# Optimization experiments

Hardware: AMD Instinct MI355X
Metric: run time of the kernel (lower is better)

The kernel has to match this reference:

```python
import jax, jax.numpy as jnp
import numpy as np

HIDDEN = 64
HALF = 32
VOCAB = 64
B, L = 256, 2048


def _l2norm(x):
    # matches torch F.normalize(dim=-1, eps=1e-12)
    return x / jnp.maximum(jnp.linalg.norm(x, axis=-1, keepdims=True), 1e-12)


def setup_inputs() -> dict:
    key = jax.random.key(0)
    ks = jax.random.split(key, 16)
    s = 0.02
    return {
        "seq": jax.random.randint(ks[0], (B, L), 0, VOCAB),
        "embed": jax.random.normal(ks[1], (VOCAB, HIDDEN), jnp.float32) * s,
        "W1": jax.random.normal(ks[2], (2 * HIDDEN, HIDDEN), jnp.float32) * s,
        "b1": jnp.zeros((2 * HIDDEN,), jnp.float32),
        "W2": jax.random.normal(ks[3], (HIDDEN, 2 * HIDDEN), jnp.float32) * s,
        "b2": jnp.zeros((HIDDEN,), jnp.float32),
        "ln_g": jnp.ones((HIDDEN,), jnp.float32),
        "ln_b": jnp.zeros((HIDDEN,), jnp.float32),
        "Ws": jax.random.normal(ks[4], (HALF, HIDDEN), jnp.float32) * s,
        "bs": jnp.zeros((HALF,), jnp.float32),
        "We": jax.random.normal(ks[5], (HALF, HIDDEN), jnp.float32) * s,
        "be": jnp.zeros((HALF,), jnp.float32),
        "Wrp": jax.random.normal(ks[6], (HIDDEN, 2 * HALF), jnp.float32) * s,
        "brp": jnp.zeros((HIDDEN,), jnp.float32),
        "Wo": jax.random.normal(ks[7], (VOCAB, HIDDEN), jnp.float32) * s,
        "bo": jnp.zeros((VOCAB,), jnp.float32),
    }


def reference(seq, embed, W1, b1, W2, b2, ln_g, ln_b, Ws, bs, We, be, Wrp, brp, Wo, bo):
    # Encoder: embed -> LayerNorm(h + FF(h))
    h0 = embed[seq]                                     # [B,L,H]
    ff = jnp.maximum(h0 @ W1.T + b1, 0.0) @ W2.T + b2
    x = h0 + ff
    mu = x.mean(-1, keepdims=True)
    var = x.var(-1, keepdims=True)
    h = (x - mu) / jnp.sqrt(var + 1e-5) * ln_g + ln_b   # [B,L,H]

    Bn, Ln, _ = h.shape
    half = Ws.shape[0]
    hs_all = h @ Ws.T + bs                              # [B,L,half]
    he_all = h @ We.T + be

    # sequential delta-rule memory writes over t = 0 .. L-2
    hs_seq = jnp.swapaxes(hs_all[:, :-1], 0, 1)         # [L-1,B,half]
    he_seq = jnp.swapaxes(he_all[:, :-1], 0, 1)
    scales = (jnp.arange(1, Ln) / Ln).astype(h.dtype)   # (t+1)/L
    M0 = jnp.zeros((Bn, half, half), h.dtype)

    def step(carry, inp):
        M_s, M_e = carry
        hs, he, sc = inp
        ks_ = _l2norm(hs)
        ke_ = _l2norm(he)
        vps = jnp.einsum('bij,bj->bi', M_s, ks_)
        vpe = jnp.einsum('bij,bj->bi', M_e, ke_)
        M_s = M_s + (hs - vps)[:, :, None] * ks_[:, None, :]
        M_e = M_e + sc * (he - vpe)[:, :, None] * ke_[:, None, :]
        return (M_s, M_e), None

    (M_s, M_e), _ = jax.lax.scan(step, (M0, M0), (hs_seq, he_seq, scales))

    # read with last-position query
    qs = _l2norm(hs_all[:, -1])
    qe = _l2norm(he_all[:, -1])
    rs = jnp.einsum('bij,bj->bi', M_s, qs)
    re = jnp.einsum('bij,bj->bi', M_e, qe)
    r = jnp.concatenate([rs, re], axis=-1)              # [B, 2*half]
    return (r @ Wrp.T + brp) @ Wo.T + bo                # [B, vocab]
```

## Files before the change

### kernel.cpp

```cpp
#include <hip/hip_runtime.h>

#define HIDDEN 64
#define HALFD  32
#define VOCAB  64
#define BATCH  256
#define SEQLEN 2048

#define RLF(v, sl) __int_as_float(__builtin_amdgcn_readlane(__float_as_int(v), (sl)))
#define RLI(v, sl) __builtin_amdgcn_readlane((v), (sl))
#define GIX(j,m) (((j)==0?0:(j)==1?7:(j)==2?13:(j)==3?18:(j)==4?22:(j)==5?25:27) + (m) - (j) - 1)
#define OM(m) (((m)*((m)+1))>>1)

__global__ __launch_bounds__(64) void vocab_kernel(
    const float* __restrict__ embed, const float* __restrict__ W1, const float* __restrict__ b1,
    const float* __restrict__ W2, const float* __restrict__ b2,
    const float* __restrict__ ln_g, const float* __restrict__ ln_b,
    const float* __restrict__ Ws, const float* __restrict__ bs,
    const float* __restrict__ We, const float* __restrict__ be,
    float* __restrict__ ws)
{
    const int v = blockIdx.x;
    const int tid = threadIdx.x;

    __shared__ float e_s[64];
    __shared__ float a1_s[128];
    __shared__ float h_s[64];

    e_s[tid] = embed[v * 64 + tid];
    __syncthreads();

    float acc0 = b1[tid], acc1 = b1[tid + 64];
    #pragma unroll 8
    for (int m = 0; m < 64; ++m) {
        float ev = e_s[m];
        acc0 = fmaf(ev, W1[tid * 64 + m], acc0);
        acc1 = fmaf(ev, W1[(tid + 64) * 64 + m], acc1);
    }
    a1_s[tid]      = fmaxf(acc0, 0.0f);
    a1_s[tid + 64] = fmaxf(acc1, 0.0f);
    __syncthreads();

    float ff = b2[tid];
    #pragma unroll 8
    for (int m = 0; m < 128; ++m) ff = fmaf(a1_s[m], W2[tid * 128 + m], ff);
    float x = e_s[tid] + ff;

    float s = x, s2 = x * x;
    #pragma unroll
    for (int off = 32; off >= 1; off >>= 1) {
        s  += __shfl_xor(s,  off, 64);
        s2 += __shfl_xor(s2, off, 64);
    }
    float mu  = s * (1.0f / 64.0f);
    float var = s2 * (1.0f / 64.0f) - mu * mu;
    float hval = (x - mu) * rsqrtf(var + 1e-5f) * ln_g[tid] + ln_b[tid];
    h_s[tid] = hval;
    __syncthreads();

    const int j = tid & 31;
    const bool is_s = tid < 32;
    const float* W = is_s ? Ws : We;
    float acc = is_s ? bs[j] : be[j];
    #pragma unroll 8
    for (int m = 0; m < 64; ++m) acc = fmaf(h_s[m], W[j * 64 + m], acc);

    float n2 = acc * acc;
    #pragma unroll
    for (int off = 16; off >= 1; off >>= 1) n2 += __shfl_xor(n2, off, 64);
    float norm = sqrtf(n2);
    float kn = acc / fmaxf(norm, 1e-12f);

    const int base = v * 32 + j;
    if (is_s) { ws[base]        = kn; ws[4096 + base] = acc; }
    else      { ws[2048 + base] = kn; ws[6144 + base] = acc; }
}

__global__ __launch_bounds__(256) void gram_kernel(float* __restrict__ ws)
{
    const int w = blockIdx.x;
    const int tid = threadIdx.x;
    __shared__ float k_s[2048];
    const float* kb = ws + w * 2048;
    for (int i = tid; i < 2048; i += 256) k_s[i] = kb[i];
    __syncthreads();
    const int a  = tid >> 2;
    const int b0 = (tid & 3) << 4;
    float* Gw = ws + 8192 + w * 4096 + a * 64;
    for (int bb = 0; bb < 16; ++bb) {
        const int bcol = b0 + bb;
        float acc = 0.f;
        #pragma unroll
        for (int m = 0; m < 32; ++m) acc = fmaf(k_s[a * 32 + m], k_s[bcol * 32 + m], acc);
        Gw[bcol] = acc;
    }
}

static __device__ __forceinline__ void build_wpack(
    const int* tj, float fb, float invL, bool is_e, bool is_last, float* Wp,
    const float* __restrict__ Gg)
{
    float f[8];
    #pragma unroll
    for (int j = 0; j < 8; ++j) f[j] = is_e ? (fb + (float)j * invL) : 1.0f;
    if (is_last) f[7] = 0.0f;

    float g[28];
    #pragma unroll
    for (int j = 0; j < 7; ++j)
        #pragma unroll
        for (int m = j + 1; m < 8; ++m) g[GIX(j, m)] = Gg[tj[j] * 64 + tj[m]];

    #pragma unroll
    for (int m = 0; m < 8; ++m) {
        float col[8];
        col[m] = f[m];
        #pragma unroll
        for (int j = 6; j >= 0; --j) {
            if (j < m) {
                float acc = 0.0f;
                #pragma unroll
                for (int p = 1; p < 8; ++p)
                    if (p > j && p <= m) acc = fmaf(g[GIX(j, p)], col[p], acc);
                col[j] = -f[j] * acc;
            }
        }
        #pragma unroll
        for (int j = 0; j < 8; ++j)
            if (j <= m) Wp[OM(m) + j] = col[j];
    }
}

struct Chunk {
    int   tokv;
    int   tk[8];
    float grow[8];
    float W[36];
};

__global__ __launch_bounds__(128) void scan_kernel(
    const int* __restrict__ seq, const float* __restrict__ ws,
    const float* __restrict__ Wrp, const float* __restrict__ brp,
    const float* __restrict__ Wo, const float* __restrict__ bo,
    float* __restrict__ out)
{
    const int b    = blockIdx.x;
    const int tid  = threadIdx.x;
    const int w    = tid >> 6;
    const int lane = tid & 63;
    const int l7   = lane & 7;
    const bool is_e = (w == 1);

    __shared__ __align__(16) float4 Wt4[9][2][256];
    __shared__ __align__(16) int    toklds[SEQLEN];
    __shared__ float wacc_s[2][64];
    __shared__ float r_s[64];
    __shared__ float t1_s[64];

    const float* Gg = ws + 8192 + w * 4096;
    const int*   sq = seq + b * SEQLEN;

    {
        const int4* sq4 = (const int4*)sq;
        int4* tl = (int4*)toklds;
        #pragma unroll
        for (int i = 0; i < 4; ++i) tl[tid + i * 128] = sq4[tid + i * 128];
    }
    __syncthreads();

    {
        const float invL = 1.0f / (float)SEQLEN;
        #pragma unroll
        for (int qq = 0; qq < 4; ++qq) {
            const int c = lane + (qq << 6);
            int tj[8];
            #pragma unroll
            for (int j = 0; j < 8; ++j) tj[j] = toklds[c * 8 + j];
            float Wp[36];
            build_wpack(tj, (float)(8 * c + 1) * invL, invL, is_e, c == 255, Wp, Gg);
            #pragma unroll
            for (int i = 0; i < 9; ++i)
                Wt4[i][w][c] = make_float4(Wp[4*i], Wp[4*i+1], Wp[4*i+2], Wp[4*i+3]);
        }
    }
    __syncthreads();

    Chunk A, B;
    float u, waccv = 0.0f;

    A.tokv = sq[2040 + l7];
    #pragma unroll
    for (int j = 0; j < 8; ++j) A.tk[j] = RLI(A.tokv, j);
    #pragma unroll
    for (int j = 0; j < 8; ++j) A.grow[j] = Gg[A.tk[j] * 64 + lane];
    #pragma unroll
    for (int i = 0; i < 9; ++i) {
        float4 v = Wt4[i][w][255];
        A.W[4*i] = v.x; A.W[4*i+1] = v.y; A.W[4*i+2] = v.z; A.W[4*i+3] = v.w;
    }
    B.tokv = sq[2032 + l7];
    u = Gg[A.tk[7] * 64 + lane];
    float braw = __shfl(u, A.tokv, 64);

    auto body = [&](Chunk& cur, Chunk& nxt, int c) {
        float t0 = RLF(braw, 0), t1 = RLF(braw, 1), t2 = RLF(braw, 2), t3 = RLF(braw, 3);
        float t4 = RLF(braw, 4), t5 = RLF(braw, 5), t6 = RLF(braw, 6), t7 = RLF(braw, 7);

        const int cm1 = (c > 0) ? c - 1 : 0;
        const int cm2 = (c > 1) ? c - 2 : 0;
        #pragma unroll
        for (int j = 0; j < 8; ++j) nxt.tk[j] = RLI(nxt.tokv, j);
        #pragma unroll
        for (int j = 0; j < 8; ++j) nxt.grow[j] = Gg[nxt.tk[j] * 64 + lane];
        #pragma unroll
        for (int i = 0; i < 9; ++i) {
            float4 v = Wt4[i][w][cm1];
            nxt.W[4*i] = v.x; nxt.W[4*i+1] = v.y; nxt.W[4*i+2] = v.z; nxt.W[4*i+3] = v.w;
        }
        int tokv2 = sq[cm2 * 8 + l7];

        const float* W = cur.W;
        float s7 = W[35] * t7;
        float s6 = fmaf(W[27], t6, W[34] * t7);
        float s5 = fmaf(W[20], t5, W[26] * t6) + W[33] * t7;
        float s4 = fmaf(W[14], t4, W[19] * t5) + fmaf(W[25], t6, W[32] * t7);
        float s3 = fmaf(W[9],  t3, W[13] * t4) + fmaf(W[18], t5, fmaf(W[24], t6, W[31] * t7));
        float s2 = fmaf(W[5],  t2, W[8]  * t3) + fmaf(W[12], t4, W[17] * t5) + fmaf(W[23], t6, W[30] * t7);
        float s1 = fmaf(W[2],  t1, W[4]  * t2) + fmaf(W[7],  t3, W[11] * t4) + fmaf(W[16], t5, fmaf(W[22], t6, W[29] * t7));
        float s0 = fmaf(W[0],  t0, W[1]  * t1) + fmaf(W[3],  t2, W[6]  * t3) + fmaf(W[10], t4, W[15] * t5) + fmaf(W[21], t6, W[28] * t7);

        float dA = fmaf(cur.grow[0], s0, fmaf(cur.grow[1], s1, fmaf(cur.grow[2], s2, cur.grow[3] * s3)));
        float dB = fmaf(cur.grow[4], s4, fmaf(cur.grow[5], s5, fmaf(cur.grow[6], s6, cur.grow[7] * s7)));
        u -= (dA + dB);

        braw = __shfl(u, nxt.tokv, 64);

        waccv += (lane == cur.tk[0]) ? s0 : 0.0f;
        waccv += (lane == cur.tk[1]) ? s1 : 0.0f;
        waccv += (lane == cur.tk[2]) ? s2 : 0.0f;
        waccv += (lane == cur.tk[3]) ? s3 : 0.0f;
        waccv += (lane == cur.tk[4]) ? s4 : 0.0f;
        waccv += (lane == cur.tk[5]) ? s5 : 0.0f;
        waccv += (lane == cur.tk[6]) ? s6 : 0.0f;
        waccv += (lane == cur.tk[7]) ? s7 : 0.0f;

        cur.tokv = tokv2;
    };

    for (int c = 255; c >= 1; c -= 2) {
        body(A, B, c);
        body(B, A, c - 1);
    }

    wacc_s[w][lane] = waccv;
    __syncthreads();

    if (tid < 64) {
        const int w2  = tid >> 5;
        const int rho = tid & 31;
        const float* vv = ws + 4096 + w2 * 2048;
        const float* wa = &wacc_s[w2][0];
        float acc = 0.0f;
        #pragma unroll 8
        for (int tok = 0; tok < 64; ++tok) acc = fmaf(wa[tok], vv[tok * 32 + rho], acc);
        r_s[tid] = acc;
    }
    __syncthreads();

    if (tid < 64) {
        float acc = brp[tid];
        #pragma unroll 8
        for (int m = 0; m < 64; ++m) acc = fmaf(Wrp[tid * 64 + m], r_s[m], acc);
        t1_s[tid] = acc;
    }
    __syncthreads();
    if (tid < 64) {
        float acc = bo[tid];
        #pragma unroll 8
        for (int m = 0; m < 64; ++m) acc = fmaf(Wo[tid * 64 + m], t1_s[m], acc);
        out[b * 64 + tid] = acc;
    }
}

extern "C" void kernel_launch(void* const* d_in, const int* in_sizes, int n_in,
                              void* d_out, int out_size, void* d_ws, size_t ws_size,
                              hipStream_t stream)
{
    const int*   seq   = (const int*)  d_in[0];
    const float* embed = (const float*)d_in[1];
    const float* W1    = (const float*)d_in[2];
    const float* b1    = (const float*)d_in[3];
    const float* W2    = (const float*)d_in[4];
    const float* b2    = (const float*)d_in[5];
    const float* ln_g  = (const float*)d_in[6];
    const float* ln_b  = (const float*)d_in[7];
    const float* Ws    = (const float*)d_in[8];
    const float* bs    = (const float*)d_in[9];
    const float* We    = (const float*)d_in[10];
    const float* be    = (const float*)d_in[11];
    const float* Wrp   = (const float*)d_in[12];
    const float* brp   = (const float*)d_in[13];
    const float* Wo    = (const float*)d_in[14];
    const float* bo    = (const float*)d_in[15];
    float* ws  = (float*)d_ws;
    float* out = (float*)d_out;

    hipLaunchKernelGGL(vocab_kernel, dim3(VOCAB), dim3(64), 0, stream,
                       embed, W1, b1, W2, b2, ln_g, ln_b, Ws, bs, We, be, ws);
    hipLaunchKernelGGL(gram_kernel, dim3(2), dim3(256), 0, stream, ws);
    hipLaunchKernelGGL(scan_kernel, dim3(BATCH), dim3(128), 0, stream,
                       seq, ws, Wrp, brp, Wo, bo, out);
}
```

Measured before the change: 200.6 us.

## Restructure chunked scan recurrence with lookahead correction and lane-parallel triangular solve

The scan loop now spreads the 8x8 triangular chunk solve across lanes: each lane holds one row of the solve matrix, stored in LDS in an XOR-swizzled layout, and the results are broadcast with readlane. The next chunk's input is gathered one step early and then corrected with the previous chunk's outputs, which takes the shuffle off the serial dependency chain. The gram kernel is split over more blocks with padded shared memory, and the small matvec loops use multiple accumulators to increase ILP. In exchange the loop does extra shuffles per step and the floating-point summation order changes.

New measurement: 190.6 us. -5.0%, faster.

```diff
diff --git a/kernel.cpp b/kernel.cpp
--- a/kernel.cpp
+++ b/kernel.cpp
@@ -29,21 +29,32 @@
     e_s[tid] = embed[v * 64 + tid];
     __syncthreads();
 
-    float acc0 = b1[tid], acc1 = b1[tid + 64];
-    #pragma unroll 8
-    for (int m = 0; m < 64; ++m) {
-        float ev = e_s[m];
-        acc0 = fmaf(ev, W1[tid * 64 + m], acc0);
-        acc1 = fmaf(ev, W1[(tid + 64) * 64 + m], acc1);
-    }
-    a1_s[tid]      = fmaxf(acc0, 0.0f);
-    a1_s[tid + 64] = fmaxf(acc1, 0.0f);
-    __syncthreads();
-
-    float ff = b2[tid];
-    #pragma unroll 8
-    for (int m = 0; m < 128; ++m) ff = fmaf(a1_s[m], W2[tid * 128 + m], ff);
-    float x = e_s[tid] + ff;
+    float p0 = b1[tid], p1 = 0.f, p2 = 0.f, p3 = 0.f;
+    float q0 = b1[tid + 64], q1 = 0.f, q2 = 0.f, q3 = 0.f;
+    #pragma unroll
+    for (int m = 0; m < 64; m += 4) {
+        p0 = fmaf(e_s[m],   W1[tid * 64 + m],     p0);
+        p1 = fmaf(e_s[m+1], W1[tid * 64 + m + 1], p1);
+        p2 = fmaf(e_s[m+2], W1[tid * 64 + m + 2], p2);
+        p3 = fmaf(e_s[m+3], W1[tid * 64 + m + 3], p3);
+        q0 = fmaf(e_s[m],   W1[(tid + 64) * 64 + m],     q0);
+        q1 = fmaf(e_s[m+1], W1[(tid + 64) * 64 + m + 1], q1);
+        q2 = fmaf(e_s[m+2], W1[(tid + 64) * 64 + m + 2], q2);
+        q3 = fmaf(e_s[m+3], W1[(tid + 64) * 64 + m + 3], q3);
+    }
+    a1_s[tid]      = fmaxf((p0 + p1) + (p2 + p3), 0.0f);
+    a1_s[tid + 64] = fmaxf((q0 + q1) + (q2 + q3), 0.0f);
+    __syncthreads();
+
+    float f0 = b2[tid], f1 = 0.f, f2 = 0.f, f3 = 0.f;
+    #pragma unroll
+    for (int m = 0; m < 128; m += 4) {
+        f0 = fmaf(a1_s[m],   W2[tid * 128 + m],     f0);
+        f1 = fmaf(a1_s[m+1], W2[tid * 128 + m + 1], f1);
+        f2 = fmaf(a1_s[m+2], W2[tid * 128 + m + 2], f2);
+        f3 = fmaf(a1_s[m+3], W2[tid * 128 + m + 3], f3);
+    }
+    float x = e_s[tid] + ((f0 + f1) + (f2 + f3));
 
     float s = x, s2 = x * x;
     #pragma unroll
@@ -60,9 +71,16 @@
     const int j = tid & 31;
     const bool is_s = tid < 32;
     const float* W = is_s ? Ws : We;
-    float acc = is_s ? bs[j] : be[j];
-    #pragma unroll 8
-    for (int m = 0; m < 64; ++m) acc = fmaf(h_s[m], W[j * 64 + m], acc);
+    float c0 = is_s ? bs[j] : be[j];
+    float c1 = 0.f, c2 = 0.f, c3 = 0.f;
+    #pragma unroll
+    for (int m = 0; m < 64; m += 4) {
+        c0 = fmaf(h_s[m],   W[j * 64 + m],     c0);
+        c1 = fmaf(h_s[m+1], W[j * 64 + m + 1], c1);
+        c2 = fmaf(h_s[m+2], W[j * 64 + m + 2], c2);
+        c3 = fmaf(h_s[m+3], W[j * 64 + m + 3], c3);
+    }
+    float acc = (c0 + c1) + (c2 + c3);
 
     float n2 = acc * acc;
     #pragma unroll
@@ -77,21 +95,26 @@
 
 __global__ __launch_bounds__(256) void gram_kernel(float* __restrict__ ws)
 {
-    const int w = blockIdx.x;
+    const int w   = blockIdx.x & 1;
+    const int seg = blockIdx.x >> 1;
     const int tid = threadIdx.x;
-    __shared__ float k_s[2048];
+    __shared__ float k_s[64][33];
     const float* kb = ws + w * 2048;
-    for (int i = tid; i < 2048; i += 256) k_s[i] = kb[i];
-    __syncthreads();
-    const int a  = tid >> 2;
-    const int b0 = (tid & 3) << 4;
+    for (int i = tid; i < 2048; i += 256) k_s[i >> 5][i & 31] = kb[i];
+    __syncthreads();
+    const int a  = seg * 16 + (tid >> 4);
+    const int b0 = (tid & 15) << 2;
     float* Gw = ws + 8192 + w * 4096 + a * 64;
-    for (int bb = 0; bb < 16; ++bb) {
+    #pragma unroll
+    for (int bb = 0; bb < 4; ++bb) {
         const int bcol = b0 + bb;
-        float acc = 0.f;
-        #pragma unroll
-        for (int m = 0; m < 32; ++m) acc = fmaf(k_s[a * 32 + m], k_s[bcol * 32 + m], acc);
-        Gw[bcol] = acc;
+        float acc0 = 0.f, acc1 = 0.f;
+        #pragma unroll
+        for (int m = 0; m < 32; m += 2) {
+            acc0 = fmaf(k_s[a][m],     k_s[bcol][m],     acc0);
+            acc1 = fmaf(k_s[a][m + 1], k_s[bcol][m + 1], acc1);
+        }
+        Gw[bcol] = acc0 + acc1;
     }
 }
 
@@ -134,7 +157,9 @@
     int   tokv;
     int   tk[8];
     float grow[8];
-    float W[36];
+    float R[8];
+    float braw;
+    float bp[8];
 };
 
 __global__ __launch_bounds__(128) void scan_kernel(
@@ -150,8 +175,8 @@
     const int l7   = lane & 7;
     const bool is_e = (w == 1);
 
-    __shared__ __align__(16) float4 Wt4[9][2][256];
-    __shared__ __align__(16) int    toklds[SEQLEN];
+    __shared__ __align__(16) float Wlds[2][256][8][8];
+    __shared__ __align__(16) int   toklds[SEQLEN];
     __shared__ float wacc_s[2][64];
     __shared__ float r_s[64];
     __shared__ float t1_s[64];
@@ -177,73 +202,100 @@
             for (int j = 0; j < 8; ++j) tj[j] = toklds[c * 8 + j];
             float Wp[36];
             build_wpack(tj, (float)(8 * c + 1) * invL, invL, is_e, c == 255, Wp, Gg);
+            const int cx = c & 7;
             #pragma unroll
-            for (int i = 0; i < 9; ++i)
-                Wt4[i][w][c] = make_float4(Wp[4*i], Wp[4*i+1], Wp[4*i+2], Wp[4*i+3]);
+            for (int i = 0; i < 8; ++i) {
+                float r[8];
+                #pragma unroll
+                for (int m = 0; m < 8; ++m) r[m] = (m >= i) ? Wp[OM(m) + i] : 0.0f;
+                float4* dst = (float4*)&Wlds[w][c][i ^ cx][0];
+                dst[0] = make_float4(r[0], r[1], r[2], r[3]);
+                dst[1] = make_float4(r[4], r[5], r[6], r[7]);
+            }
         }
     }
     __syncthreads();
 
     Chunk A, B;
-    float u, waccv = 0.0f;
+    float u, wacc0 = 0.0f, wacc1 = 0.0f;
+    float sp0, sp1, sp2, sp3, sp4, sp5, sp6, sp7;
 
     A.tokv = sq[2040 + l7];
+    B.tokv = sq[2032 + l7];
+    int tv2 = sq[2024 + l7];
     #pragma unroll
     for (int j = 0; j < 8; ++j) A.tk[j] = RLI(A.tokv, j);
     #pragma unroll
     for (int j = 0; j < 8; ++j) A.grow[j] = Gg[A.tk[j] * 64 + lane];
-    #pragma unroll
-    for (int i = 0; i < 9; ++i) {
-        float4 v = Wt4[i][w][255];
-        A.W[4*i] = v.x; A.W[4*i+1] = v.y; A.W[4*i+2] = v.z; A.W[4*i+3] = v.w;
-    }
-    B.tokv = sq[2032 + l7];
+    {
+        const float4* rp = (const float4*)&Wlds[w][255][l7 ^ 7][0];
+        float4 lo = rp[0], hi = rp[1];
+        A.R[0] = lo.x; A.R[1] = lo.y; A.R[2] = lo.z; A.R[3] = lo.w;
+        A.R[4] = hi.x; A.R[5] = hi.y; A.R[6] = hi.z; A.R[7] = hi.w;
+    }
     u = Gg[A.tk[7] * 64 + lane];
-    float braw = __shfl(u, A.tokv, 64);
+    A.braw = __shfl(u, A.tokv, 64);
+    B.braw = __shfl(u, B.tokv, 64);
+    #pragma unroll
+    for (int j = 0; j < 8; ++j) {
+        A.bp[j] = 0.0f;
+        B.bp[j] = __shfl(A.grow[j], B.tokv, 64);
+    }
+    sp0 = sp1 = sp2 = sp3 = sp4 = sp5 = sp6 = sp7 = 0.0f;
 
     auto body = [&](Chunk& cur, Chunk& nxt, int c) {
-        float t0 = RLF(braw, 0), t1 = RLF(braw, 1), t2 = RLF(braw, 2), t3 = RLF(braw, 3);
-        float t4 = RLF(braw, 4), t5 = RLF(braw, 5), t6 = RLF(braw, 6), t7 = RLF(braw, 7);
-
         const int cm1 = (c > 0) ? c - 1 : 0;
-        const int cm2 = (c > 1) ? c - 2 : 0;
+        const int cm3 = (c > 2) ? c - 3 : 0;
+
+        float c01 = fmaf(cur.bp[1], sp1, cur.bp[0] * sp0);
+        float c23 = fmaf(cur.bp[3], sp3, cur.bp[2] * sp2);
+        float c45 = fmaf(cur.bp[5], sp5, cur.bp[4] * sp4);
+        float c67 = fmaf(cur.bp[7], sp7, cur.bp[6] * sp6);
+        float tl = cur.braw - ((c01 + c23) + (c45 + c67));
+        float t0 = RLF(tl, 0), t1 = RLF(tl, 1), t2 = RLF(tl, 2), t3 = RLF(tl, 3);
+        float t4 = RLF(tl, 4), t5 = RLF(tl, 5), t6 = RLF(tl, 6), t7 = RLF(tl, 7);
+
         #pragma unroll
         for (int j = 0; j < 8; ++j) nxt.tk[j] = RLI(nxt.tokv, j);
         #pragma unroll
         for (int j = 0; j < 8; ++j) nxt.grow[j] = Gg[nxt.tk[j] * 64 + lane];
-        #pragma unroll
-        for (int i = 0; i < 9; ++i) {
-            float4 v = Wt4[i][w][cm1];
-            nxt.W[4*i] = v.x; nxt.W[4*i+1] = v.y; nxt.W[4*i+2] = v.z; nxt.W[4*i+3] = v.w;
+        {
+            const float4* rp = (const float4*)&Wlds[w][cm1][l7 ^ (cm1 & 7)][0];
+            float4 lo = rp[0], hi = rp[1];
+            nxt.R[0] = lo.x; nxt.R[1] = lo.y; nxt.R[2] = lo.z; nxt.R[3] = lo.w;
+            nxt.R[4] = hi.x; nxt.R[5] = hi.y; nxt.R[6] = hi.z; nxt.R[7] = hi.w;
         }
-        int tokv2 = sq[cm2 * 8 + l7];
-
-        const float* W = cur.W;
-        float s7 = W[35] * t7;
-        float s6 = fmaf(W[27], t6, W[34] * t7);
-        float s5 = fmaf(W[20], t5, W[26] * t6) + W[33] * t7;
-        float s4 = fmaf(W[14], t4, W[19] * t5) + fmaf(W[25], t6, W[32] * t7);
-        float s3 = fmaf(W[9],  t3, W[13] * t4) + fmaf(W[18], t5, fmaf(W[24], t6, W[31] * t7));
-        float s2 = fmaf(W[5],  t2, W[8]  * t3) + fmaf(W[12], t4, W[17] * t5) + fmaf(W[23], t6, W[30] * t7);
-        float s1 = fmaf(W[2],  t1, W[4]  * t2) + fmaf(W[7],  t3, W[11] * t4) + fmaf(W[16], t5, fmaf(W[22], t6, W[29] * t7));
-        float s0 = fmaf(W[0],  t0, W[1]  * t1) + fmaf(W[3],  t2, W[6]  * t3) + fmaf(W[10], t4, W[15] * t5) + fmaf(W[21], t6, W[28] * t7);
+        int tv3 = sq[cm3 * 8 + l7];
+
+        const float* R = cur.R;
+        float a0 = fmaf(R[1], t1, R[0] * t0);
+        float a1 = fmaf(R[3], t3, R[2] * t2);
+        float a2 = fmaf(R[5], t5, R[4] * t4);
+        float a3 = fmaf(R[7], t7, R[6] * t6);
+        float sd = (a0 + a1) + (a2 + a3);
+        float s0 = RLF(sd, 0), s1 = RLF(sd, 1), s2 = RLF(sd, 2), s3 = RLF(sd, 3);
+        float s4 = RLF(sd, 4), s5 = RLF(sd, 5), s6 = RLF(sd, 6), s7 = RLF(sd, 7);
 
         float dA = fmaf(cur.grow[0], s0, fmaf(cur.grow[1], s1, fmaf(cur.grow[2], s2, cur.grow[3] * s3)));
         float dB = fmaf(cur.grow[4], s4, fmaf(cur.grow[5], s5, fmaf(cur.grow[6], s6, cur.grow[7] * s7)));
         u -= (dA + dB);
-
-        braw = __shfl(u, nxt.tokv, 64);
-
-        waccv += (lane == cur.tk[0]) ? s0 : 0.0f;
-        waccv += (lane == cur.tk[1]) ? s1 : 0.0f;
-        waccv += (lane == cur.tk[2]) ? s2 : 0.0f;
-        waccv += (lane == cur.tk[3]) ? s3 : 0.0f;
-        waccv += (lane == cur.tk[4]) ? s4 : 0.0f;
-        waccv += (lane == cur.tk[5]) ? s5 : 0.0f;
-        waccv += (lane == cur.tk[6]) ? s6 : 0.0f;
-        waccv += (lane == cur.tk[7]) ? s7 : 0.0f;
-
-        cur.tokv = tokv2;
+        cur.braw = __shfl(u, tv2, 64);
+        #pragma unroll
+        for (int j = 0; j < 8; ++j)
+            nxt.bp[j] = __shfl(cur.grow[j], nxt.tokv, 64);
+
+        wacc0 += (lane == cur.tk[0]) ? s0 : 0.0f;
+        wacc1 += (lane == cur.tk[1]) ? s1 : 0.0f;
+        wacc0 += (lane == cur.tk[2]) ? s2 : 0.0f;
+        wacc1 += (lane == cur.tk[3]) ? s3 : 0.0f;
+        wacc0 += (lane == cur.tk[4]) ? s4 : 0.0f;
+        wacc1 += (lane == cur.tk[5]) ? s5 : 0.0f;
+        wacc0 += (lane == cur.tk[6]) ? s6 : 0.0f;
+        wacc1 += (lane == cur.tk[7]) ? s7 : 0.0f;
+
+        cur.tokv = tv2; tv2 = tv3;
+        sp0 = s0; sp1 = s1; sp2 = s2; sp3 = s3;
+        sp4 = s4; sp5 = s5; sp6 = s6; sp7 = s7;
     };
 
     for (int c = 255; c >= 1; c -= 2) {
@@ -251,7 +303,7 @@
         body(B, A, c - 1);
     }
 
-    wacc_s[w][lane] = waccv;
+    wacc_s[w][lane] = wacc0 + wacc1;
     __syncthreads();
 
     if (tid < 64) {
@@ -306,7 +358,7 @@
 
     hipLaunchKernelGGL(vocab_kernel, dim3(VOCAB), dim3(64), 0, stream,
                        embed, W1, b1, W2, b2, ln_g, ln_b, Ws, bs, We, be, ws);
-    hipLaunchKernelGGL(gram_kernel, dim3(2), dim3(256), 0, stream, ws);
+    hipLaunchKernelGGL(gram_kernel, dim3(8), dim3(256), 0, stream, ws);
     hipLaunchKernelGGL(scan_kernel, dim3(BATCH), dim3(128), 0, stream,
                        seq, ws, Wrp, brp, Wo, bo, out);
 }
```
